# Kernel tuning notes

Hardware: AMD Instinct MI355X
Metric: run time of the kernel (lower is better)

## Reference

```python
import jax, jax.numpy as jnp
import numpy as np
from jax.scipy.special import gammaln

MAX_POS = 4096
NUM_HEADS = 8
TEMP = 1.0        # gumbel-sigmoid (RelaxedBernoulli) temperature
THRESHOLD = 0.5   # hard-boundary threshold
PRIOR = 0.2       # binomial prior on boundary rate


def setup_inputs() -> dict:
    key = jax.random.key(0)
    ks = jax.random.split(key, 6)
    B, S, D = 8, 4096, 1024
    lim = (6.0 / (D + D)) ** 0.5  # xavier_uniform for square [D,D] weights
    return {
        "hidden": jax.random.normal(ks[0], (B, S, D), jnp.float32),
        "pos_emb": 0.02 * jax.random.normal(ks[1], (MAX_POS, D), jnp.float32),
        "Wq": jax.random.uniform(ks[2], (D, D), jnp.float32, -lim, lim),
        "Wk": jax.random.uniform(ks[3], (D, D), jnp.float32, -lim, lim),
        "sig_temp": jnp.ones((1,), jnp.float32),    # sigmoid_temperature param
        "sig_thr": jnp.zeros((1,), jnp.float32),    # sigmoid_threshold param
        "noise_u": jax.random.uniform(ks[4], (B, S), jnp.float32),
    }


def reference(hidden, pos_emb, Wq, Wk, sig_temp, sig_thr, noise_u):
    B, S, D = hidden.shape
    scale = (D // NUM_HEADS) ** -0.5
    dt = hidden.dtype

    # add positional embeddings, then L2-normalize (F.normalize eps=1e-12)
    h = hidden + pos_emb[:S][None]
    h = h / jnp.maximum(jnp.linalg.norm(h, axis=-1, keepdims=True), 1e-12)

    Q = h @ Wq.T  # [B,S,D]
    K = h @ Wk.T  # [B,S,D]

    # full QK^T masked to only (i, i-1) survivors + row-sum == adjacent dots
    adj = jnp.einsum('bsd,bsd->bs', Q[:, 1:], K[:, :-1]) * scale  # [B,S-1]
    boundary_scores = jnp.concatenate([jnp.zeros((B, 1), dt), adj], axis=1)

    probs = jax.nn.sigmoid((boundary_scores - sig_thr) / sig_temp)
    probs = jnp.clip(probs, 0.0, 1.0)
    probs = probs.at[:, 0].set(1.0)

    # RelaxedBernoulli rsample (torch clamp_probs uses finfo.eps)
    eps = jnp.finfo(dt).eps
    p = jnp.clip(probs, eps, 1.0 - eps)
    logits = jnp.log(p) - jnp.log1p(-p)
    u = jnp.clip(noise_u, eps, 1.0 - eps)
    logistic = jnp.log(u) - jnp.log1p(-u)
    soft = jax.nn.sigmoid((logits + logistic) / TEMP)

    # straight-through hard boundaries
    hard = (soft > THRESHOLD).astype(dt)
    hard = jax.lax.stop_gradient(hard - soft) + soft

    # delete(hard_boundaries, hidden): segment mean-pooling between boundaries,
    # padded to S segments (jit-static shape)
    seg = jnp.clip(jnp.cumsum(hard, axis=1).astype(jnp.int32) - 1, 0, S - 1)  # [B,S]
    sums = jax.vmap(lambda ids, x: jax.ops.segment_sum(x, ids, num_segments=S))(seg, h)
    cnts = jax.vmap(lambda ids: jax.ops.segment_sum(jnp.ones((S,), dt), ids, num_segments=S))(seg)
    pooled = sums / jnp.maximum(cnts, 1.0)[..., None]  # [B,S,D]
    pooled = jnp.transpose(pooled, (1, 0, 2))          # [S,B,D]

    # binomial prior loss on boundary counts
    n = jnp.asarray(S, dt)
    k = jnp.sum(hard, axis=-1)
    log_prob = (gammaln(n + 1.0) - gammaln(k + 1.0) - gammaln(n - k + 1.0)
                + k * jnp.log(PRIOR) + (n - k) * jnp.log1p(-PRIOR))
    loss = -jnp.mean(log_prob) / n
    return pooled, loss
```

## Files before the change

### kernel.cpp

```cpp
#include <hip/hip_runtime.h>
#include <stdint.h>

namespace {

constexpr int Bb = 8, S = 4096, D = 1024, BS = 32768;
constexpr float SCALE = 0.08838834764831845f;
constexpr float FEPS  = 1.1920928955078125e-07f;
constexpr int MAXF = 4096;

typedef unsigned short u16;
typedef __attribute__((ext_vector_type(8))) _Float16 f16x8;
typedef __attribute__((ext_vector_type(4))) float    f32x4;

__device__ __forceinline__ u16 f2h(float f) {
  _Float16 h = (_Float16)f;
  return __builtin_bit_cast(u16, h);
}
__device__ __forceinline__ float h2f(u16 u) {
  return (float)__builtin_bit_cast(_Float16, u);
}
__device__ __forceinline__ void gload_lds16(const void* g, void* l) {
  __builtin_amdgcn_global_load_lds((const __attribute__((address_space(1))) void*)g,
                                   (__attribute__((address_space(3))) void*)l, 16, 0, 0);
}
#define VMCNT(n) asm volatile("s_waitcnt vmcnt(" #n ")" ::: "memory")

__global__ void prep_h(const float* __restrict__ hidden, const float* __restrict__ pos,
                       u16* __restrict__ Hf, int* __restrict__ fcnt) {
  if (blockIdx.x == 0 && threadIdx.x == 0) *fcnt = 0;
  const int r = blockIdx.x;
  const int t = threadIdx.x;
  const float4 hv = ((const float4*)(hidden + (size_t)r * D))[t];
  const float4 pv = ((const float4*)(pos + (size_t)(r & (S - 1)) * D))[t];
  float x0 = hv.x + pv.x, x1 = hv.y + pv.y, x2 = hv.z + pv.z, x3 = hv.w + pv.w;
  float ss = x0 * x0 + x1 * x1 + x2 * x2 + x3 * x3;
  #pragma unroll
  for (int m = 1; m < 64; m <<= 1) ss += __shfl_xor(ss, m, 64);
  __shared__ float red[4];
  if ((t & 63) == 0) red[t >> 6] = ss;
  __syncthreads();
  const float nrm = fmaxf(sqrtf(red[0] + red[1] + red[2] + red[3]), 1e-12f);
  ((ushort4*)(Hf + (size_t)r * D))[t] = make_ushort4(
      f2h(x0 / nrm), f2h(x1 / nrm), f2h(x2 / nrm), f2h(x3 / nrm));
}

__global__ void gemm_G(const float* __restrict__ Wq, const float* __restrict__ Wk,
                       float* __restrict__ Gf32, u16* __restrict__ Gf16) {
  __shared__ float Qs[32][64];
  __shared__ float Ks[32][64];
  const int t = threadIdx.x;
  const int i0 = blockIdx.x * 64, j0 = blockIdx.y * 64;
  const int tx = t & 15, ty = t >> 4;
  float acc[4][4] = {};
  for (int k0 = 0; k0 < D; k0 += 32) {
    #pragma unroll
    for (int q = 0; q < 2; ++q) {
      const int c = t + q * 256;
      const int row = c >> 4, c4 = (c & 15) << 2;
      *(float4*)&Qs[row][c4] = *(const float4*)&Wq[(size_t)(k0 + row) * D + i0 + c4];
      *(float4*)&Ks[row][c4] = *(const float4*)&Wk[(size_t)(k0 + row) * D + j0 + c4];
    }
    __syncthreads();
    #pragma unroll 8
    for (int kk = 0; kk < 32; ++kk) {
      const float4 qa = *(const float4*)&Qs[kk][tx << 2];
      const float4 kb = *(const float4*)&Ks[kk][ty << 2];
      const float qq[4] = {qa.x, qa.y, qa.z, qa.w};
      const float kv[4] = {kb.x, kb.y, kb.z, kb.w};
      #pragma unroll
      for (int a = 0; a < 4; ++a)
        #pragma unroll
        for (int bj = 0; bj < 4; ++bj) acc[a][bj] = fmaf(qq[a], kv[bj], acc[a][bj]);
    }
    __syncthreads();
  }
  #pragma unroll
  for (int a = 0; a < 4; ++a) {
    const int i = i0 + (tx << 2) + a;
    const size_t base = (size_t)i * D + j0 + (ty << 2);
    *(float4*)&Gf32[base] = make_float4(acc[a][0], acc[a][1], acc[a][2], acc[a][3]);
    *(ushort4*)&Gf16[base] = make_ushort4(
        f2h(acc[a][0]), f2h(acc[a][1]), f2h(acc[a][2]), f2h(acc[a][3]));
  }
}

__global__ __launch_bounds__(512, 2) void gemm_main(
    const u16* __restrict__ Hf, const u16* __restrict__ Gf,
    float* __restrict__ adj_part) {
  __shared__ u16 AbufS[3][16384];
  __shared__ u16 BbufS[3][8192];
  __shared__ float adjp[4][256];

  const int tid = threadIdx.x;
  const int bid = blockIdx.x;
  const int swz = (bid & 7) * 128 + (bid >> 3);
  const int mt = swz >> 3, nt = swz & 7;
  const int r0 = mt << 8;
  const int n0g = nt << 7;

  const int wave = tid >> 6, lane = tid & 63;
  const int wr = wave >> 2;
  const int wc = wave & 3;
  const int frow = lane & 15;
  const int fgrp = lane >> 4;
  const int sw = (lane & 7) << 4;
  const int cb0 = (fgrp * 16) ^ sw;
  const int cb1 = (64 + fgrp * 16) ^ sw;
  const int Abase = (wr * 128 + frow) * 128;
  const int Bbase = (wc * 32 + frow) * 128;

  const int trow = tid >> 3;
  const int scb = ((tid & 7) << 4) ^ ((trow & 7) << 4);
  const char* Asrc = (const char*)Hf + (size_t)(r0 + trow) * 2048 + scb;
  const char* Bsrc = (const char*)Gf + (size_t)(n0g + trow) * 2048 + scb;
  const int dst16 = tid * 16;

  f32x4 acc[8][2];
  #pragma unroll
  for (int m = 0; m < 8; ++m) { acc[m][0] = (f32x4){0,0,0,0}; acc[m][1] = (f32x4){0,0,0,0}; }

  auto stageA = [&](int b, int kt, int q) {
    gload_lds16(Asrc + (size_t)q * 131072 + (size_t)kt * 128,
                (char*)&AbufS[b][0] + q * 8192 + dst16);
  };
  auto stageB = [&](int b, int kt, int q) {
    gload_lds16(Bsrc + (size_t)q * 131072 + (size_t)kt * 128,
                (char*)&BbufS[b][0] + q * 8192 + dst16);
  };

  auto do_tile = [&](int cur, int nb, int kt, bool dostage) {
    const char* Ab = (const char*)&AbufS[cur][0];
    const char* Bb = (const char*)&BbufS[cur][0];
    f16x8 b00 = *(const f16x8*)(Bb + Bbase + cb0);
    f16x8 b01 = *(const f16x8*)(Bb + Bbase + cb1);
    f16x8 b10 = *(const f16x8*)(Bb + Bbase + 2048 + cb0);
    f16x8 b11 = *(const f16x8*)(Bb + Bbase + 2048 + cb1);
    {
      f16x8 a0k0 = *(const f16x8*)(Ab + Abase + 0 * 2048 + cb0);
      f16x8 a0k1 = *(const f16x8*)(Ab + Abase + 0 * 2048 + cb1);
      f16x8 a1k0 = *(const f16x8*)(Ab + Abase + 1 * 2048 + cb0);
      f16x8 a1k1 = *(const f16x8*)(Ab + Abase + 1 * 2048 + cb1);
      f16x8 a2k0 = *(const f16x8*)(Ab + Abase + 2 * 2048 + cb0);
      f16x8 a2k1 = *(const f16x8*)(Ab + Abase + 2 * 2048 + cb1);
      f16x8 a3k0 = *(const f16x8*)(Ab + Abase + 3 * 2048 + cb0);
      f16x8 a3k1 = *(const f16x8*)(Ab + Abase + 3 * 2048 + cb1);
      if (dostage) { stageA(nb, kt + 2, 0); stageA(nb, kt + 2, 1); stageA(nb, kt + 2, 2); }
      __builtin_amdgcn_s_setprio(1);
      acc[0][0] = __builtin_amdgcn_mfma_f32_16x16x32_f16(a0k0, b00, acc[0][0], 0, 0, 0);
      acc[0][0] = __builtin_amdgcn_mfma_f32_16x16x32_f16(a0k1, b01, acc[0][0], 0, 0, 0);
      acc[0][1] = __builtin_amdgcn_mfma_f32_16x16x32_f16(a0k0, b10, acc[0][1], 0, 0, 0);
      acc[0][1] = __builtin_amdgcn_mfma_f32_16x16x32_f16(a0k1, b11, acc[0][1], 0, 0, 0);
      acc[1][0] = __builtin_amdgcn_mfma_f32_16x16x32_f16(a1k0, b00, acc[1][0], 0, 0, 0);
      acc[1][0] = __builtin_amdgcn_mfma_f32_16x16x32_f16(a1k1, b01, acc[1][0], 0, 0, 0);
      acc[1][1] = __builtin_amdgcn_mfma_f32_16x16x32_f16(a1k0, b10, acc[1][1], 0, 0, 0);
      acc[1][1] = __builtin_amdgcn_mfma_f32_16x16x32_f16(a1k1, b11, acc[1][1], 0, 0, 0);
      acc[2][0] = __builtin_amdgcn_mfma_f32_16x16x32_f16(a2k0, b00, acc[2][0], 0, 0, 0);
      acc[2][0] = __builtin_amdgcn_mfma_f32_16x16x32_f16(a2k1, b01, acc[2][0], 0, 0, 0);
      acc[2][1] = __builtin_amdgcn_mfma_f32_16x16x32_f16(a2k0, b10, acc[2][1], 0, 0, 0);
      acc[2][1] = __builtin_amdgcn_mfma_f32_16x16x32_f16(a2k1, b11, acc[2][1], 0, 0, 0);
      acc[3][0] = __builtin_amdgcn_mfma_f32_16x16x32_f16(a3k0, b00, acc[3][0], 0, 0, 0);
      acc[3][0] = __builtin_amdgcn_mfma_f32_16x16x32_f16(a3k1, b01, acc[3][0], 0, 0, 0);
      acc[3][1] = __builtin_amdgcn_mfma_f32_16x16x32_f16(a3k0, b10, acc[3][1], 0, 0, 0);
      acc[3][1] = __builtin_amdgcn_mfma_f32_16x16x32_f16(a3k1, b11, acc[3][1], 0, 0, 0);
      __builtin_amdgcn_s_setprio(0);
    }
    {
      f16x8 a4k0 = *(const f16x8*)(Ab + Abase + 4 * 2048 + cb0);
      f16x8 a4k1 = *(const f16x8*)(Ab + Abase + 4 * 2048 + cb1);
      f16x8 a5k0 = *(const f16x8*)(Ab + Abase + 5 * 2048 + cb0);
      f16x8 a5k1 = *(const f16x8*)(Ab + Abase + 5 * 2048 + cb1);
      f16x8 a6k0 = *(const f16x8*)(Ab + Abase + 6 * 2048 + cb0);
      f16x8 a6k1 = *(const f16x8*)(Ab + Abase + 6 * 2048 + cb1);
      f16x8 a7k0 = *(const f16x8*)(Ab + Abase + 7 * 2048 + cb0);
      f16x8 a7k1 = *(const f16x8*)(Ab + Abase + 7 * 2048 + cb1);
      if (dostage) { stageA(nb, kt + 2, 3); stageB(nb, kt + 2, 0); stageB(nb, kt + 2, 1); }
      __builtin_amdgcn_s_setprio(1);
      acc[4][0] = __builtin_amdgcn_mfma_f32_16x16x32_f16(a4k0, b00, acc[4][0], 0, 0, 0);
      acc[4][0] = __builtin_amdgcn_mfma_f32_16x16x32_f16(a4k1, b01, acc[4][0], 0, 0, 0);
      acc[4][1] = __builtin_amdgcn_mfma_f32_16x16x32_f16(a4k0, b10, acc[4][1], 0, 0, 0);
      acc[4][1] = __builtin_amdgcn_mfma_f32_16x16x32_f16(a4k1, b11, acc[4][1], 0, 0, 0);
      acc[5][0] = __builtin_amdgcn_mfma_f32_16x16x32_f16(a5k0, b00, acc[5][0], 0, 0, 0);
      acc[5][0] = __builtin_amdgcn_mfma_f32_16x16x32_f16(a5k1, b01, acc[5][0], 0, 0, 0);
      acc[5][1] = __builtin_amdgcn_mfma_f32_16x16x32_f16(a5k0, b10, acc[5][1], 0, 0, 0);
      acc[5][1] = __builtin_amdgcn_mfma_f32_16x16x32_f16(a5k1, b11, acc[5][1], 0, 0, 0);
      acc[6][0] = __builtin_amdgcn_mfma_f32_16x16x32_f16(a6k0, b00, acc[6][0], 0, 0, 0);
      acc[6][0] = __builtin_amdgcn_mfma_f32_16x16x32_f16(a6k1, b01, acc[6][0], 0, 0, 0);
      acc[6][1] = __builtin_amdgcn_mfma_f32_16x16x32_f16(a6k0, b10, acc[6][1], 0, 0, 0);
      acc[6][1] = __builtin_amdgcn_mfma_f32_16x16x32_f16(a6k1, b11, acc[6][1], 0, 0, 0);
      acc[7][0] = __builtin_amdgcn_mfma_f32_16x16x32_f16(a7k0, b00, acc[7][0], 0, 0, 0);
      acc[7][0] = __builtin_amdgcn_mfma_f32_16x16x32_f16(a7k1, b01, acc[7][0], 0, 0, 0);
      acc[7][1] = __builtin_amdgcn_mfma_f32_16x16x32_f16(a7k0, b10, acc[7][1], 0, 0, 0);
      acc[7][1] = __builtin_amdgcn_mfma_f32_16x16x32_f16(a7k1, b11, acc[7][1], 0, 0, 0);
      __builtin_amdgcn_s_setprio(0);
    }
  };

  stageA(0, 0, 0); stageA(0, 0, 1); stageA(0, 0, 2); stageA(0, 0, 3);
  stageB(0, 0, 0); stageB(0, 0, 1);
  stageA(1, 1, 0); stageA(1, 1, 1); stageA(1, 1, 2); stageA(1, 1, 3);
  stageB(1, 1, 0); stageB(1, 1, 1);

  int cur = 0;
  #pragma unroll 1
  for (int kt = 0; kt < 14; ++kt) {
    const int nb = (cur >= 1) ? cur - 1 : 2;
    VMCNT(6);
    __builtin_amdgcn_s_barrier();
    __builtin_amdgcn_sched_barrier(0);
    do_tile(cur, nb, kt, true);
    cur = (cur == 2) ? 0 : cur + 1;
  }
  VMCNT(6);
  __builtin_amdgcn_s_barrier();
  __builtin_amdgcn_sched_barrier(0);
  do_tile(cur, 0, 14, false);
  cur = (cur == 2) ? 0 : cur + 1;
  VMCNT(0);
  __builtin_amdgcn_s_barrier();
  __builtin_amdgcn_sched_barrier(0);
  do_tile(cur, 0, 15, false);

  #pragma unroll
  for (int m = 0; m < 8; ++m) {
    #pragma unroll
    for (int reg = 0; reg < 4; ++reg) {
      const int rl = wr * 128 + m * 16 + fgrp * 4 + reg;
      const int gr = r0 + rl;
      float sum = 0.f;
      if (((gr + 1) & (S - 1)) != 0) {
        const u16* hrow = Hf + (size_t)(gr + 1) * D + n0g + wc * 32 + frow;
        sum = acc[m][0][reg] * h2f(hrow[0]) + acc[m][1][reg] * h2f(hrow[16]);
      }
      #pragma unroll
      for (int off = 1; off < 16; off <<= 1) sum += __shfl_xor(sum, off, 64);
      if (frow == 0) adjp[wc][rl] = sum;
    }
  }
  __syncthreads();
  if (tid < 256) {
    adj_part[(size_t)nt * BS + r0 + tid] =
        adjp[0][tid] + adjp[1][tid] + adjp[2][tid] + adjp[3][tid];
  }
}

__global__ void score_flag(const float* __restrict__ adj_part,
                           const float* __restrict__ sig_temp, const float* __restrict__ sig_thr,
                           const float* __restrict__ noise_u,
                           unsigned char* __restrict__ hard, int* __restrict__ flags,
                           int* __restrict__ fcnt) {
  const int idx = blockIdx.x * 256 + threadIdx.x;
  const int s = idx & (S - 1);
  float sc = 0.f;
  if (s > 0) {
    float a = 0.f;
    #pragma unroll
    for (int p = 0; p < 8; ++p) a += adj_part[(size_t)p * BS + idx - 1];
    sc = a * SCALE;
  }
  const float temp = sig_temp[0], thr = sig_thr[0];
  float pr = 1.f / (1.f + expf(-(sc - thr) / temp));
  pr = fminf(fmaxf(pr, 0.f), 1.f);
  if (s == 0) pr = 1.f;
  const float p = fminf(fmaxf(pr, FEPS), 1.f - FEPS);
  const float lgt = logf(p) - log1pf(-p);
  const float uu = fminf(fmaxf(noise_u[idx], FEPS), 1.f - FEPS);
  const float lgs = logf(uu) - log1pf(-uu);
  const float z = lgt + lgs;
  hard[idx] = (z > 0.f) ? 1 : 0;
  if (s > 0 && fabsf(z) < 1e-3f) {
    const int k = atomicAdd(fcnt, 1);
    if (k < MAXF) flags[k] = idx;
  }
}

__global__ __launch_bounds__(256) void fixup_part(const int* __restrict__ flags,
    const int* __restrict__ fcnt, const float* __restrict__ hidden,
    const float* __restrict__ pos, const float* __restrict__ Gf32,
    float* __restrict__ pz) {
  __shared__ float h0s[1024];
  __shared__ float h1s[1024];
  __shared__ float red[4];
  const int t = threadIdx.x;
  const int slice = blockIdx.x & 7;
  const int nf = min(*fcnt, MAXF);
  for (int w = blockIdx.x >> 3; w < nf; w += 32) {
    const int idx = flags[w];
    #pragma unroll
    for (int rr = 0; rr < 2; ++rr) {
      const int r = idx - 1 + rr;
      float* hs = rr ? h1s : h0s;
      const float4 hv = ((const float4*)(hidden + (size_t)r * D))[t];
      const float4 pv = ((const float4*)(pos + (size_t)(r & (S - 1)) * D))[t];
      const float x0 = hv.x + pv.x, x1 = hv.y + pv.y, x2 = hv.z + pv.z, x3 = hv.w + pv.w;
      float ss = x0 * x0 + x1 * x1 + x2 * x2 + x3 * x3;
      #pragma unroll
      for (int m = 1; m < 64; m <<= 1) ss += __shfl_xor(ss, m, 64);
      __syncthreads();
      if ((t & 63) == 0) red[t >> 6] = ss;
      __syncthreads();
      const float nrm = fmaxf(sqrtf(red[0] + red[1] + red[2] + red[3]), 1e-12f);
      hs[4 * t + 0] = x0 / nrm; hs[4 * t + 1] = x1 / nrm;
      hs[4 * t + 2] = x2 / nrm; hs[4 * t + 3] = x3 / nrm;
    }
    __syncthreads();
    const float4 h0v = *(const float4*)&h0s[t << 2];
    float acc = 0.f;
    const int i0 = slice << 7;
    #pragma unroll 4
    for (int i = i0; i < i0 + 128; ++i) {
      const float4 g = ((const float4*)(Gf32 + (size_t)i * D))[t];
      const float d = g.x * h0v.x + g.y * h0v.y + g.z * h0v.z + g.w * h0v.w;
      acc = fmaf(h1s[i], d, acc);
    }
    #pragma unroll
    for (int m = 1; m < 64; m <<= 1) acc += __shfl_xor(acc, m, 64);
    __syncthreads();
    if ((t & 63) == 0) red[t >> 6] = acc;
    __syncthreads();
    if (t == 0) pz[(size_t)w * 8 + slice] = red[0] + red[1] + red[2] + red[3];
    __syncthreads();
  }
}

__global__ void fixup_final(const int* __restrict__ flags, const int* __restrict__ fcnt,
    const float* __restrict__ pz,
    const float* __restrict__ sig_temp, const float* __restrict__ sig_thr,
    const float* __restrict__ noise_u, unsigned char* __restrict__ hard) {
  const int w = blockIdx.x * 256 + threadIdx.x;
  const int nf = min(*fcnt, MAXF);
  if (w >= nf) return;
  const int idx = flags[w];
  float a = 0.f;
  #pragma unroll
  for (int p = 0; p < 8; ++p) a += pz[(size_t)w * 8 + p];
  const float sc = a * SCALE;
  const float temp = sig_temp[0], thr = sig_thr[0];
  float pr = 1.f / (1.f + expf(-(sc - thr) / temp));
  pr = fminf(fmaxf(pr, 0.f), 1.f);
  const float p = fminf(fmaxf(pr, FEPS), 1.f - FEPS);
  const float lgt = logf(p) - log1pf(-p);
  const float uu = fminf(fmaxf(noise_u[idx], FEPS), 1.f - FEPS);
  const float lgs = logf(uu) - log1pf(-uu);
  hard[idx] = ((lgt + lgs) > 0.f) ? 1 : 0;
}

__global__ void decide_scan(const unsigned char* __restrict__ hard_,
                            int* __restrict__ seg_start, int* __restrict__ nseg_out,
                            float* __restrict__ kf_out) {
  const int b = blockIdx.x, t = threadIdx.x;
  __shared__ int ssum[256];
  const uint4 hv = ((const uint4*)(hard_ + (size_t)b * S))[t];
  const uint32_t wds[4] = {hv.x, hv.y, hv.z, hv.w};
  const uint32_t bsum = hv.x + hv.y + hv.z + hv.w;
  const int loc = (int)((bsum & 255) + ((bsum >> 8) & 255) +
                        ((bsum >> 16) & 255) + (bsum >> 24));
  ssum[t] = loc;
  __syncthreads();
  for (int off = 1; off < 256; off <<= 1) {
    int v = ssum[t];
    if (t >= off) v += ssum[t - off];
    __syncthreads();
    ssum[t] = v;
    __syncthreads();
  }
  const int ktot = ssum[255];
  int cum = ssum[t] - loc;
  #pragma unroll
  for (int e = 0; e < 16; ++e) {
    const int s = (t << 4) + e;
    const int bit = (int)((wds[e >> 2] >> ((e & 3) * 8)) & 1);
    const int pseg = min(max(cum - 1, 0), S - 1);
    cum += bit;
    const int seg = min(max(cum - 1, 0), S - 1);
    if (s == 0 || seg != pseg) seg_start[b * S + seg] = s;
  }
  if (t == 0) {
    nseg_out[b] = min(max(ktot, 1), S);
    kf_out[b] = (float)ktot;
  }
}

__global__ void pool(const u16* __restrict__ Hf,
                     const int* __restrict__ seg_start, const int* __restrict__ nseg_arr,
                     float* __restrict__ out) {
  const int j = blockIdx.x, b = blockIdx.y, t = threadIdx.x;
  const int ns = nseg_arr[b];
  float4* o = (float4*)(out + (((size_t)j * Bb + b) << 10));
  if (j >= ns) {
    o[t] = (float4){0.f, 0.f, 0.f, 0.f};
    return;
  }
  const int s0 = seg_start[b * S + j];
  const int s1 = (j + 1 < ns) ? seg_start[b * S + j + 1] : S;
  float a0 = 0.f, a1 = 0.f, a2 = 0.f, a3 = 0.f;
  for (int s = s0; s < s1; ++s) {
    const ushort4 hv = *(const ushort4*)(Hf + (((size_t)b * S + s) << 10) + (t << 2));
    a0 += h2f(hv.x); a1 += h2f(hv.y); a2 += h2f(hv.z); a3 += h2f(hv.w);
  }
  const float c = (float)(s1 - s0);
  o[t] = (float4){a0 / c, a1 / c, a2 / c, a3 / c};
}

__global__ void loss_k(const float* __restrict__ kf, float* __restrict__ out) {
  const int t = threadIdx.x;
  float lp = 0.f;
  if (t < 8) {
    const float n = 4096.f;
    const float k = kf[t];
    lp = lgammaf(n + 1.f) - lgammaf(k + 1.f) - lgammaf(n - k + 1.f)
       + k * logf(0.2f) + (n - k) * log1pf(-0.2f);
  }
  #pragma unroll
  for (int off = 1; off < 8; off <<= 1) lp += __shfl_xor(lp, off, 64);
  if (t == 0) out[(size_t)BS * 1024] = -(lp / 8.f) / 4096.f;
}

}

extern "C" void kernel_launch(void* const* d_in, const int* in_sizes, int n_in,
                              void* d_out, int out_size, void* d_ws, size_t ws_size,
                              hipStream_t stream) {
  (void)in_sizes; (void)n_in; (void)out_size; (void)ws_size;
  const float* hidden = (const float*)d_in[0];
  const float* pos    = (const float*)d_in[1];
  const float* Wq     = (const float*)d_in[2];
  const float* Wk     = (const float*)d_in[3];
  const float* stemp  = (const float*)d_in[4];
  const float* sthr   = (const float*)d_in[5];
  const float* nois   = (const float*)d_in[6];
  float* out = (float*)d_out;
  char* ws = (char*)d_ws;

  u16*   Hf        = (u16*)(ws);
  u16*   Gf16      = (u16*)(ws + 67108864);
  float* Gf32      = (float*)(ws + 69206016);
  float* adj_part  = (float*)(ws + 73400320);
  unsigned char* hard = (unsigned char*)(ws + 74448896);
  int*   flags     = (int*)(ws + 74481664);
  float* pz        = (float*)(ws + 74498048);
  int*   fcnt      = (int*)(ws + 74629120);
  int*   seg_start = (int*)(ws + 74629184);
  int*   nseg      = (int*)(ws + 74760256);
  float* kf        = (float*)(ws + 74760320);

  hipLaunchKernelGGL(prep_h,      dim3(BS),       dim3(256), 0, stream, hidden, pos, Hf, fcnt);
  hipLaunchKernelGGL(gemm_G,      dim3(16, 16),   dim3(256), 0, stream, Wq, Wk, Gf32, Gf16);
  hipLaunchKernelGGL(gemm_main,   dim3(1024),     dim3(512), 0, stream, Hf, Gf16, adj_part);
  hipLaunchKernelGGL(score_flag,  dim3(BS/256),   dim3(256), 0, stream, adj_part, stemp, sthr, nois, hard, flags, fcnt);
  hipLaunchKernelGGL(fixup_part,  dim3(256),      dim3(256), 0, stream, flags, fcnt, hidden, pos, Gf32, pz);
  hipLaunchKernelGGL(fixup_final, dim3(MAXF/256), dim3(256), 0, stream, flags, fcnt, pz, stemp, sthr, nois, hard);
  hipLaunchKernelGGL(decide_scan, dim3(Bb),       dim3(256), 0, stream, hard, seg_start, nseg, kf);
  hipLaunchKernelGGL(pool,        dim3(S, Bb),    dim3(256), 0, stream, Hf, seg_start, nseg, out);
  hipLaunchKernelGGL(loss_k,      dim3(1),        dim3(64),  0, stream, kf, out);
}
```

Measured before the change: 278.8 us.

## Widen main GEMM tile to 256x256 and split-K the weight product

The main f16 MFMA GEMM tile goes from 256x128 to 256x256, halving the block count and the adj_part partial columns. Its 3-stage staggered pipeline becomes a simpler 2-buffer double-buffered loop that waits for all loads before each tile. The small Wq^T·Wk GEMM is split across 4 K-slices with a separate combine kernel, to raise parallelism on a launch of only 256 blocks. The cost is more accumulator registers per thread (128 floats), higher LDS use, less load/compute overlap from the full vmcnt wait, and an extra kernel launch plus partial-sum traffic.

Measured after the change: 236.4 us. -15.2%, faster.

```diff
diff --git a/kernel.cpp b/kernel.cpp
--- a/kernel.cpp
+++ b/kernel.cpp
@@ -44,15 +44,16 @@
       f2h(x0 / nrm), f2h(x1 / nrm), f2h(x2 / nrm), f2h(x3 / nrm));
 }
 
-__global__ void gemm_G(const float* __restrict__ Wq, const float* __restrict__ Wk,
-                       float* __restrict__ Gf32, u16* __restrict__ Gf16) {
+__global__ void gemm_G_part(const float* __restrict__ Wq, const float* __restrict__ Wk,
+                            float* __restrict__ Gpart) {
   __shared__ float Qs[32][64];
   __shared__ float Ks[32][64];
   const int t = threadIdx.x;
   const int i0 = blockIdx.x * 64, j0 = blockIdx.y * 64;
+  const int kz = blockIdx.z * 256;
   const int tx = t & 15, ty = t >> 4;
   float acc[4][4] = {};
-  for (int k0 = 0; k0 < D; k0 += 32) {
+  for (int k0 = kz; k0 < kz + 256; k0 += 32) {
     #pragma unroll
     for (int q = 0; q < 2; ++q) {
       const int c = t + q * 256;
@@ -74,29 +75,41 @@
     }
     __syncthreads();
   }
+  float* gp = Gpart + (size_t)blockIdx.z * 1048576;
   #pragma unroll
   for (int a = 0; a < 4; ++a) {
     const int i = i0 + (tx << 2) + a;
-    const size_t base = (size_t)i * D + j0 + (ty << 2);
-    *(float4*)&Gf32[base] = make_float4(acc[a][0], acc[a][1], acc[a][2], acc[a][3]);
-    *(ushort4*)&Gf16[base] = make_ushort4(
-        f2h(acc[a][0]), f2h(acc[a][1]), f2h(acc[a][2]), f2h(acc[a][3]));
-  }
+    *(float4*)&gp[(size_t)i * D + j0 + (ty << 2)] =
+        make_float4(acc[a][0], acc[a][1], acc[a][2], acc[a][3]);
+  }
+}
+
+__global__ void gemm_G_comb(const float* __restrict__ Gpart,
+                            float* __restrict__ Gf32, u16* __restrict__ Gf16) {
+  const size_t e = ((size_t)blockIdx.x * 256 + threadIdx.x) * 4;
+  float4 a = *(const float4*)&Gpart[e];
+  #pragma unroll
+  for (int z = 1; z < 4; ++z) {
+    const float4 p = *(const float4*)&Gpart[(size_t)z * 1048576 + e];
+    a.x += p.x; a.y += p.y; a.z += p.z; a.w += p.w;
+  }
+  *(float4*)&Gf32[e] = a;
+  *(ushort4*)&Gf16[e] = make_ushort4(f2h(a.x), f2h(a.y), f2h(a.z), f2h(a.w));
 }
 
 __global__ __launch_bounds__(512, 2) void gemm_main(
     const u16* __restrict__ Hf, const u16* __restrict__ Gf,
     float* __restrict__ adj_part) {
-  __shared__ u16 AbufS[3][16384];
-  __shared__ u16 BbufS[3][8192];
+  __shared__ u16 Abuf[2][16384];
+  __shared__ u16 Bbuf[2][16384];
   __shared__ float adjp[4][256];
 
   const int tid = threadIdx.x;
   const int bid = blockIdx.x;
-  const int swz = (bid & 7) * 128 + (bid >> 3);
-  const int mt = swz >> 3, nt = swz & 7;
+  const int swz = (bid & 7) * 64 + (bid >> 3);
+  const int mt = swz >> 2, nt = swz & 3;
   const int r0 = mt << 8;
-  const int n0g = nt << 7;
+  const int n0g = nt << 8;
 
   const int wave = tid >> 6, lane = tid & 63;
   const int wr = wave >> 2;
@@ -107,7 +120,7 @@
   const int cb0 = (fgrp * 16) ^ sw;
   const int cb1 = (64 + fgrp * 16) ^ sw;
   const int Abase = (wr * 128 + frow) * 128;
-  const int Bbase = (wc * 32 + frow) * 128;
+  const int Bbase = (wc * 64 + frow) * 128;
 
   const int trow = tid >> 3;
   const int scb = ((tid & 7) << 4) ^ ((trow & 7) << 4);
@@ -115,110 +128,53 @@
   const char* Bsrc = (const char*)Gf + (size_t)(n0g + trow) * 2048 + scb;
   const int dst16 = tid * 16;
 
-  f32x4 acc[8][2];
-  #pragma unroll
-  for (int m = 0; m < 8; ++m) { acc[m][0] = (f32x4){0,0,0,0}; acc[m][1] = (f32x4){0,0,0,0}; }
-
-  auto stageA = [&](int b, int kt, int q) {
-    gload_lds16(Asrc + (size_t)q * 131072 + (size_t)kt * 128,
-                (char*)&AbufS[b][0] + q * 8192 + dst16);
+  f32x4 acc[8][4];
+  #pragma unroll
+  for (int m = 0; m < 8; ++m)
+    #pragma unroll
+    for (int n = 0; n < 4; ++n) acc[m][n] = (f32x4){0.f, 0.f, 0.f, 0.f};
+
+  auto stage = [&](int b, int kt) {
+    #pragma unroll
+    for (int q = 0; q < 4; ++q) {
+      gload_lds16(Asrc + (size_t)q * 131072 + (size_t)kt * 128,
+                  (char*)&Abuf[b][0] + q * 8192 + dst16);
+      gload_lds16(Bsrc + (size_t)q * 131072 + (size_t)kt * 128,
+                  (char*)&Bbuf[b][0] + q * 8192 + dst16);
+    }
   };
-  auto stageB = [&](int b, int kt, int q) {
-    gload_lds16(Bsrc + (size_t)q * 131072 + (size_t)kt * 128,
-                (char*)&BbufS[b][0] + q * 8192 + dst16);
+
+  auto compute = [&](int b) {
+    const char* Ab = (const char*)&Abuf[b][0];
+    const char* Bp = (const char*)&Bbuf[b][0];
+    #pragma unroll
+    for (int ks = 0; ks < 2; ++ks) {
+      const int cb = ks ? cb1 : cb0;
+      f16x8 bf[4], af[8];
+      #pragma unroll
+      for (int n = 0; n < 4; ++n) bf[n] = *(const f16x8*)(Bp + Bbase + n * 2048 + cb);
+      #pragma unroll
+      for (int m = 0; m < 8; ++m) af[m] = *(const f16x8*)(Ab + Abase + m * 2048 + cb);
+      __builtin_amdgcn_s_setprio(1);
+      #pragma unroll
+      for (int m = 0; m < 8; ++m)
+        #pragma unroll
+        for (int n = 0; n < 4; ++n)
+          acc[m][n] = __builtin_amdgcn_mfma_f32_16x16x32_f16(af[m], bf[n], acc[m][n], 0, 0, 0);
+      __builtin_amdgcn_s_setprio(0);
+    }
   };
 
-  auto do_tile = [&](int cur, int nb, int kt, bool dostage) {
-    const char* Ab = (const char*)&AbufS[cur][0];
-    const char* Bb = (const char*)&BbufS[cur][0];
-    f16x8 b00 = *(const f16x8*)(Bb + Bbase + cb0);
-    f16x8 b01 = *(const f16x8*)(Bb + Bbase + cb1);
-    f16x8 b10 = *(const f16x8*)(Bb + Bbase + 2048 + cb0);
-    f16x8 b11 = *(const f16x8*)(Bb + Bbase + 2048 + cb1);
-    {
-      f16x8 a0k0 = *(const f16x8*)(Ab + Abase + 0 * 2048 + cb0);
-      f16x8 a0k1 = *(const f16x8*)(Ab + Abase + 0 * 2048 + cb1);
-      f16x8 a1k0 = *(const f16x8*)(Ab + Abase + 1 * 2048 + cb0);
-      f16x8 a1k1 = *(const f16x8*)(Ab + Abase + 1 * 2048 + cb1);
-      f16x8 a2k0 = *(const f16x8*)(Ab + Abase + 2 * 2048 + cb0);
-      f16x8 a2k1 = *(const f16x8*)(Ab + Abase + 2 * 2048 + cb1);
-      f16x8 a3k0 = *(const f16x8*)(Ab + Abase + 3 * 2048 + cb0);
-      f16x8 a3k1 = *(const f16x8*)(Ab + Abase + 3 * 2048 + cb1);
-      if (dostage) { stageA(nb, kt + 2, 0); stageA(nb, kt + 2, 1); stageA(nb, kt + 2, 2); }
-      __builtin_amdgcn_s_setprio(1);
-      acc[0][0] = __builtin_amdgcn_mfma_f32_16x16x32_f16(a0k0, b00, acc[0][0], 0, 0, 0);
-      acc[0][0] = __builtin_amdgcn_mfma_f32_16x16x32_f16(a0k1, b01, acc[0][0], 0, 0, 0);
-      acc[0][1] = __builtin_amdgcn_mfma_f32_16x16x32_f16(a0k0, b10, acc[0][1], 0, 0, 0);
-      acc[0][1] = __builtin_amdgcn_mfma_f32_16x16x32_f16(a0k1, b11, acc[0][1], 0, 0, 0);
-      acc[1][0] = __builtin_amdgcn_mfma_f32_16x16x32_f16(a1k0, b00, acc[1][0], 0, 0, 0);
-      acc[1][0] = __builtin_amdgcn_mfma_f32_16x16x32_f16(a1k1, b01, acc[1][0], 0, 0, 0);
-      acc[1][1] = __builtin_amdgcn_mfma_f32_16x16x32_f16(a1k0, b10, acc[1][1], 0, 0, 0);
-      acc[1][1] = __builtin_amdgcn_mfma_f32_16x16x32_f16(a1k1, b11, acc[1][1], 0, 0, 0);
-      acc[2][0] = __builtin_amdgcn_mfma_f32_16x16x32_f16(a2k0, b00, acc[2][0], 0, 0, 0);
-      acc[2][0] = __builtin_amdgcn_mfma_f32_16x16x32_f16(a2k1, b01, acc[2][0], 0, 0, 0);
-      acc[2][1] = __builtin_amdgcn_mfma_f32_16x16x32_f16(a2k0, b10, acc[2][1], 0, 0, 0);
-      acc[2][1] = __builtin_amdgcn_mfma_f32_16x16x32_f16(a2k1, b11, acc[2][1], 0, 0, 0);
-      acc[3][0] = __builtin_amdgcn_mfma_f32_16x16x32_f16(a3k0, b00, acc[3][0], 0, 0, 0);
-      acc[3][0] = __builtin_amdgcn_mfma_f32_16x16x32_f16(a3k1, b01, acc[3][0], 0, 0, 0);
-      acc[3][1] = __builtin_amdgcn_mfma_f32_16x16x32_f16(a3k0, b10, acc[3][1], 0, 0, 0);
-      acc[3][1] = __builtin_amdgcn_mfma_f32_16x16x32_f16(a3k1, b11, acc[3][1], 0, 0, 0);
-      __builtin_amdgcn_s_setprio(0);
-    }
-    {
-      f16x8 a4k0 = *(const f16x8*)(Ab + Abase + 4 * 2048 + cb0);
-      f16x8 a4k1 = *(const f16x8*)(Ab + Abase + 4 * 2048 + cb1);
-      f16x8 a5k0 = *(const f16x8*)(Ab + Abase + 5 * 2048 + cb0);
-      f16x8 a5k1 = *(const f16x8*)(Ab + Abase + 5 * 2048 + cb1);
-      f16x8 a6k0 = *(const f16x8*)(Ab + Abase + 6 * 2048 + cb0);
-      f16x8 a6k1 = *(const f16x8*)(Ab + Abase + 6 * 2048 + cb1);
-      f16x8 a7k0 = *(const f16x8*)(Ab + Abase + 7 * 2048 + cb0);
-      f16x8 a7k1 = *(const f16x8*)(Ab + Abase + 7 * 2048 + cb1);
-      if (dostage) { stageA(nb, kt + 2, 3); stageB(nb, kt + 2, 0); stageB(nb, kt + 2, 1); }
-      __builtin_amdgcn_s_setprio(1);
-      acc[4][0] = __builtin_amdgcn_mfma_f32_16x16x32_f16(a4k0, b00, acc[4][0], 0, 0, 0);
-      acc[4][0] = __builtin_amdgcn_mfma_f32_16x16x32_f16(a4k1, b01, acc[4][0], 0, 0, 0);
-      acc[4][1] = __builtin_amdgcn_mfma_f32_16x16x32_f16(a4k0, b10, acc[4][1], 0, 0, 0);
-      acc[4][1] = __builtin_amdgcn_mfma_f32_16x16x32_f16(a4k1, b11, acc[4][1], 0, 0, 0);
-      acc[5][0] = __builtin_amdgcn_mfma_f32_16x16x32_f16(a5k0, b00, acc[5][0], 0, 0, 0);
-      acc[5][0] = __builtin_amdgcn_mfma_f32_16x16x32_f16(a5k1, b01, acc[5][0], 0, 0, 0);
-      acc[5][1] = __builtin_amdgcn_mfma_f32_16x16x32_f16(a5k0, b10, acc[5][1], 0, 0, 0);
-      acc[5][1] = __builtin_amdgcn_mfma_f32_16x16x32_f16(a5k1, b11, acc[5][1], 0, 0, 0);
-      acc[6][0] = __builtin_amdgcn_mfma_f32_16x16x32_f16(a6k0, b00, acc[6][0], 0, 0, 0);
-      acc[6][0] = __builtin_amdgcn_mfma_f32_16x16x32_f16(a6k1, b01, acc[6][0], 0, 0, 0);
-      acc[6][1] = __builtin_amdgcn_mfma_f32_16x16x32_f16(a6k0, b10, acc[6][1], 0, 0, 0);
-      acc[6][1] = __builtin_amdgcn_mfma_f32_16x16x32_f16(a6k1, b11, acc[6][1], 0, 0, 0);
-      acc[7][0] = __builtin_amdgcn_mfma_f32_16x16x32_f16(a7k0, b00, acc[7][0], 0, 0, 0);
-      acc[7][0] = __builtin_amdgcn_mfma_f32_16x16x32_f16(a7k1, b01, acc[7][0], 0, 0, 0);
-      acc[7][1] = __builtin_amdgcn_mfma_f32_16x16x32_f16(a7k0, b10, acc[7][1], 0, 0, 0);
-      acc[7][1] = __builtin_amdgcn_mfma_f32_16x16x32_f16(a7k1, b11, acc[7][1], 0, 0, 0);
-      __builtin_amdgcn_s_setprio(0);
-    }
-  };
-
-  stageA(0, 0, 0); stageA(0, 0, 1); stageA(0, 0, 2); stageA(0, 0, 3);
-  stageB(0, 0, 0); stageB(0, 0, 1);
-  stageA(1, 1, 0); stageA(1, 1, 1); stageA(1, 1, 2); stageA(1, 1, 3);
-  stageB(1, 1, 0); stageB(1, 1, 1);
-
-  int cur = 0;
+  stage(0, 0);
   #pragma unroll 1
-  for (int kt = 0; kt < 14; ++kt) {
-    const int nb = (cur >= 1) ? cur - 1 : 2;
-    VMCNT(6);
+  for (int t = 0; t < 16; ++t) {
+    VMCNT(0);
     __builtin_amdgcn_s_barrier();
     __builtin_amdgcn_sched_barrier(0);
-    do_tile(cur, nb, kt, true);
-    cur = (cur == 2) ? 0 : cur + 1;
-  }
-  VMCNT(6);
-  __builtin_amdgcn_s_barrier();
-  __builtin_amdgcn_sched_barrier(0);
-  do_tile(cur, 0, 14, false);
-  cur = (cur == 2) ? 0 : cur + 1;
-  VMCNT(0);
-  __builtin_amdgcn_s_barrier();
-  __builtin_amdgcn_sched_barrier(0);
-  do_tile(cur, 0, 15, false);
+    if (t < 15) stage((t + 1) & 1, t + 1);
+    __builtin_amdgcn_sched_barrier(0);
+    compute(t & 1);
+  }
 
   #pragma unroll
   for (int m = 0; m < 8; ++m) {
@@ -228,8 +184,10 @@
       const int gr = r0 + rl;
       float sum = 0.f;
       if (((gr + 1) & (S - 1)) != 0) {
-        const u16* hrow = Hf + (size_t)(gr + 1) * D + n0g + wc * 32 + frow;
-        sum = acc[m][0][reg] * h2f(hrow[0]) + acc[m][1][reg] * h2f(hrow[16]);
+        const u16* hrow = Hf + (size_t)(gr + 1) * D + n0g + wc * 64 + frow;
+        #pragma unroll
+        for (int n = 0; n < 4; ++n)
+          sum = fmaf(acc[m][n][reg], h2f(hrow[n * 16]), sum);
       }
       #pragma unroll
       for (int off = 1; off < 16; off <<= 1) sum += __shfl_xor(sum, off, 64);
@@ -254,7 +212,7 @@
   if (s > 0) {
     float a = 0.f;
     #pragma unroll
-    for (int p = 0; p < 8; ++p) a += adj_part[(size_t)p * BS + idx - 1];
+    for (int p = 0; p < 4; ++p) a += adj_part[(size_t)p * BS + idx - 1];
     sc = a * SCALE;
   }
   const float temp = sig_temp[0], thr = sig_thr[0];
@@ -442,14 +400,16 @@
   int*   seg_start = (int*)(ws + 74629184);
   int*   nseg      = (int*)(ws + 74760256);
   float* kf        = (float*)(ws + 74760320);
-
-  hipLaunchKernelGGL(prep_h,      dim3(BS),       dim3(256), 0, stream, hidden, pos, Hf, fcnt);
-  hipLaunchKernelGGL(gemm_G,      dim3(16, 16),   dim3(256), 0, stream, Wq, Wk, Gf32, Gf16);
-  hipLaunchKernelGGL(gemm_main,   dim3(1024),     dim3(512), 0, stream, Hf, Gf16, adj_part);
-  hipLaunchKernelGGL(score_flag,  dim3(BS/256),   dim3(256), 0, stream, adj_part, stemp, sthr, nois, hard, flags, fcnt);
-  hipLaunchKernelGGL(fixup_part,  dim3(256),      dim3(256), 0, stream, flags, fcnt, hidden, pos, Gf32, pz);
-  hipLaunchKernelGGL(fixup_final, dim3(MAXF/256), dim3(256), 0, stream, flags, fcnt, pz, stemp, sthr, nois, hard);
-  hipLaunchKernelGGL(decide_scan, dim3(Bb),       dim3(256), 0, stream, hard, seg_start, nseg, kf);
-  hipLaunchKernelGGL(pool,        dim3(S, Bb),    dim3(256), 0, stream, Hf, seg_start, nseg, out);
-  hipLaunchKernelGGL(loss_k,      dim3(1),        dim3(64),  0, stream, kf, out);
-}
+  float* Gpart     = (float*)(ws + 74760384);
+
+  hipLaunchKernelGGL(prep_h,      dim3(BS),         dim3(256), 0, stream, hidden, pos, Hf, fcnt);
+  hipLaunchKernelGGL(gemm_G_part, dim3(16, 16, 4),  dim3(256), 0, stream, Wq, Wk, Gpart);
+  hipLaunchKernelGGL(gemm_G_comb, dim3(1024),       dim3(256), 0, stream, Gpart, Gf32, Gf16);
+  hipLaunchKernelGGL(gemm_main,   dim3(512),        dim3(512), 0, stream, Hf, Gf16, adj_part);
+  hipLaunchKernelGGL(score_flag,  dim3(BS/256),     dim3(256), 0, stream, adj_part, stemp, sthr, nois, hard, flags, fcnt);
+  hipLaunchKernelGGL(fixup_part,  dim3(256),        dim3(256), 0, stream, flags, fcnt, hidden, pos, Gf32, pz);
+  hipLaunchKernelGGL(fixup_final, dim3(MAXF/256),   dim3(256), 0, stream, flags, fcnt, pz, stemp, sthr, nois, hard);
+  hipLaunchKernelGGL(decide_scan, dim3(Bb),         dim3(256), 0, stream, hard, seg_start, nseg, kf);
+  hipLaunchKernelGGL(pool,        dim3(S, Bb),      dim3(256), 0, stream, Hf, seg_start, nseg, out);
+  hipLaunchKernelGGL(loss_k,      dim3(1),          dim3(64),  0, stream, kf, out);
+}
```
